# Optimization experiments

Hardware: AMD Instinct MI355X
Metric: run time of the kernel (lower is better)

Reference implementation:

```python
import jax, jax.numpy as jnp
import numpy as np

N_NODES = 50000
N_EDGES = 800000
IN_CH = 64
EDGE_DIM = 8
HIDDEN = 128
NUM_GRAPHS = 256


def setup_inputs() -> dict:
    key = jax.random.key(0)
    ks = jax.random.split(key, 16)
    x = jax.random.normal(ks[0], (N_NODES, IN_CH), dtype=jnp.float32)
    edge_index = jax.random.randint(ks[1], (2, N_EDGES), 0, N_NODES, dtype=jnp.int64)
    edge_attr = jax.random.normal(ks[2], (N_EDGES, EDGE_DIM), dtype=jnp.float32)
    batch = jnp.sort(jax.random.randint(ks[3], (N_NODES,), 0, NUM_GRAPHS, dtype=jnp.int64))

    def lin(k, fan_in, fan_out):
        bound = 1.0 / np.sqrt(fan_in)
        kw, kb = jax.random.split(k)
        W = jax.random.uniform(kw, (fan_in, fan_out), minval=-bound, maxval=bound, dtype=jnp.float32)
        b = jax.random.uniform(kb, (fan_out,), minval=-bound, maxval=bound, dtype=jnp.float32)
        return W, b

    W1, b1 = lin(ks[4], IN_CH, HIDDEN)
    We1, be1 = lin(ks[5], EDGE_DIM, IN_CH)
    W2, b2 = lin(ks[6], HIDDEN, HIDDEN)
    We2, be2 = lin(ks[7], EDGE_DIM, HIDDEN)
    W3, b3 = lin(ks[8], HIDDEN, HIDDEN)
    We3, be3 = lin(ks[9], EDGE_DIM, HIDDEN)
    return {"x": x, "edge_index": edge_index, "edge_attr": edge_attr, "batch": batch,
            "W1": W1, "b1": b1, "We1": We1, "be1": be1,
            "W2": W2, "b2": b2, "We2": We2, "be2": be2,
            "W3": W3, "b3": b3, "We3": We3, "be3": be3}


def gine_conv(x, src, dst, edge_attr, W, b, We, be):
    # edge feature projection to node-feature dim, then message = relu(x_j + e)
    e = edge_attr @ We + be                      # [E, d]
    msg = jax.nn.relu(x[src] + e)                # [E, d]
    agg = jax.ops.segment_sum(msg, dst, num_segments=x.shape[0])  # [N, d]
    # eps = 0 (PyG default, not trainable)
    return (x + agg) @ W + b


def reference(x, edge_index, edge_attr, batch,
              W1, b1, We1, be1, W2, b2, We2, be2, W3, b3, We3, be3):
    x = x.astype(jnp.float32)
    edge_attr = edge_attr.astype(jnp.float32)
    src, dst = edge_index[0], edge_index[1]
    x = jax.nn.relu(gine_conv(x, src, dst, edge_attr, W1, b1, We1, be1))
    x = jax.nn.relu(gine_conv(x, src, dst, edge_attr, W2, b2, We2, be2))
    x = jax.nn.relu(gine_conv(x, src, dst, edge_attr, W3, b3, We3, be3))
    # global mean pool over graphs
    sums = jax.ops.segment_sum(x, batch, num_segments=NUM_GRAPHS)          # [G, d]
    counts = jax.ops.segment_sum(jnp.ones((x.shape[0],), x.dtype), batch, num_segments=NUM_GRAPHS)
    return sums / jnp.maximum(counts, 1.0)[:, None]
```

## Files before the change

### kernel.cpp

```cpp
#include <hip/hip_runtime.h>
#include <hip/hip_bf16.h>
#include <hip/hip_fp16.h>

#define N_NODES 50000
#define N_EDGES 800000
#define IN_CH 64
#define EDGE_DIM 8
#define HIDDEN 128
#define NUM_GRAPHS 256
#define QSCALE 256.0f
#define QINV   (1.0f / 256.0f)

typedef __attribute__((ext_vector_type(8))) _Float16 half8;
typedef __attribute__((ext_vector_type(4))) float floatx4;
typedef __attribute__((ext_vector_type(2))) float floatx2;
typedef __attribute__((ext_vector_type(4))) int intx4;

static __device__ __forceinline__ __half2 u2h(int u) {
    union { int i; __half2 h; } cv; cv.i = u; return cv.h;
}
static __device__ __forceinline__ int h2u(__half2 h) {
    union { __half2 h; int i; } cv; cv.h = h; return cv.i;
}
static __device__ __forceinline__ unsigned short h1u(__half h) {
    union { __half h; unsigned short u; } cv; cv.h = h; return cv.u;
}
static __device__ __forceinline__ unsigned char f32_to_fp8(float v) {
    int pk = __builtin_amdgcn_cvt_pk_fp8_f32(v, v, 0, false);
    return (unsigned char)(pk & 0xff);
}

#define XH_ELEMS (N_NODES * IN_CH)

__global__ __launch_bounds__(256) void hist_cvt_kernel(
    const int* __restrict__ dst, int* __restrict__ deg,
    const float* __restrict__ x, unsigned char* __restrict__ xh8,
    const float* __restrict__ W1, const float* __restrict__ W2,
    const float* __restrict__ W3,
    _Float16* __restrict__ Wt1, _Float16* __restrict__ Wt2,
    _Float16* __restrict__ Wt3, int E)
{
    int i = blockIdx.x * blockDim.x + threadIdx.x;
    if (i < E) atomicAdd(&deg[dst[i]], 1);
    int idx = i;
    if (idx < XH_ELEMS) { xh8[idx] = f32_to_fp8(x[idx]); return; }
    idx -= XH_ELEMS;
    if (idx < 128 * IN_CH) {
        int n = idx / IN_CH, k = idx - n * IN_CH;
        Wt1[idx] = (_Float16)W1[k * 128 + n];
        return;
    }
    idx -= 128 * IN_CH;
    if (idx < 128 * HIDDEN) {
        int n = idx / HIDDEN, k = idx - n * HIDDEN;
        Wt2[idx] = (_Float16)W2[k * 128 + n];
        return;
    }
    idx -= 128 * HIDDEN;
    if (idx < 128 * HIDDEN) {
        int n = idx / HIDDEN, k = idx - n * HIDDEN;
        Wt3[idx] = (_Float16)W3[k * 128 + n];
    }
}

__global__ __launch_bounds__(256) void scan1_kernel(
    const int* __restrict__ deg, int* __restrict__ incl,
    int* __restrict__ blockSums, int N)
{
    __shared__ int s[256];
    int b = blockIdx.x, t = threadIdx.x;
    int i0 = b * 512 + 2 * t;
    int a0 = (i0 < N) ? deg[i0] : 0;
    int a1 = (i0 + 1 < N) ? deg[i0 + 1] : 0;
    int ps = a0 + a1;
    s[t] = ps;
    __syncthreads();
    for (int off = 1; off < 256; off <<= 1) {
        int v = (t >= off) ? s[t - off] : 0;
        __syncthreads();
        s[t] += v;
        __syncthreads();
    }
    int exclp = s[t] - ps;
    if (i0 < N)     incl[i0]     = exclp + a0;
    if (i0 + 1 < N) incl[i0 + 1] = exclp + a0 + a1;
    if (t == 255) blockSums[b] = s[255];
}

__global__ __launch_bounds__(128) void scan2_kernel(int* __restrict__ blockSums, int B)
{
    __shared__ int s[128];
    int t = threadIdx.x;
    int v = (t < B) ? blockSums[t] : 0;
    s[t] = v;
    __syncthreads();
    for (int off = 1; off < 128; off <<= 1) {
        int u = (t >= off) ? s[t - off] : 0;
        __syncthreads();
        s[t] += u;
        __syncthreads();
    }
    if (t < B) blockSums[t] = s[t] - v;
}

__global__ __launch_bounds__(256) void scan3_kernel(
    const int* __restrict__ incl, const int* __restrict__ deg,
    const int* __restrict__ blockSums, int* __restrict__ rowptr,
    int* __restrict__ pos, int N)
{
    int i = blockIdx.x * blockDim.x + threadIdx.x;
    if (i >= N) return;
    int v = incl[i] - deg[i] + blockSums[i >> 9];
    rowptr[i] = v;
    pos[i] = v;
}

__global__ __launch_bounds__(256) void scatter_rec_kernel(
    const int* __restrict__ dst, const int* __restrict__ src,
    const float* __restrict__ ea, int* __restrict__ pos,
    int* __restrict__ src_s, __half* __restrict__ ea16, int E)
{
    int e = blockIdx.x * blockDim.x + threadIdx.x;
    if (e >= E) return;
    int d = dst[e];
    int p = atomicAdd(&pos[d], 1);
    __builtin_nontemporal_store(src[e], &src_s[p]);
    const float4* q = (const float4*)(ea + (size_t)e * EDGE_DIM);
    float4 a = q[0], b = q[1];
    intx4 r;
    r.x = h2u(__floats2half2_rn(a.x, a.y));
    r.y = h2u(__floats2half2_rn(a.z, a.w));
    r.z = h2u(__floats2half2_rn(b.x, b.y));
    r.w = h2u(__floats2half2_rn(b.z, b.w));
    __builtin_nontemporal_store(r, (intx4*)(ea16 + (size_t)p * EDGE_DIM));
}

#define BF 8

__global__ __launch_bounds__(256) void gather_xs128_kernel(
    const unsigned char* __restrict__ h8,
    const int*    __restrict__ src_s,
    const __half* __restrict__ ea16,
    const int*    __restrict__ rowptr,
    const int*    __restrict__ deg,
    const float*  __restrict__ We,
    const float*  __restrict__ be,
    __half*       __restrict__ xs,
    int N)
{
    int wave = threadIdx.x >> 6;
    int n    = blockIdx.x * 4 + wave;
    if (n >= N) return;
    int l  = threadIdx.x & 63;
    int j0 = 2 * l;

    __half2 hw[8];
    #pragma unroll
    for (int k = 0; k < 8; ++k) {
        float2 wv = *(const float2*)&We[k * 128 + j0];
        hw[k] = __floats2half2_rn(wv.x, wv.y);
    }
    float2 bevf = *(const float2*)&be[j0];
    __half2 bev2 = __floats2half2_rn(bevf.x, bevf.y);

    int start = __builtin_amdgcn_readfirstlane(rowptr[n]);
    int dg    = __builtin_amdgcn_readfirstlane(deg[n]);

    unsigned short selfraw = *(const unsigned short*)&h8[(size_t)n * 128 + j0];
    floatx2 hf = __builtin_amdgcn_cvt_pk_f32_fp8((int)selfraw, false);
    int acci0 = 0, acci1 = 0;

    int nb = dg / BF;
    int base = start;
    for (int b = 0; b < nb; ++b, base += BF) {
        int sid[BF];
        #pragma unroll
        for (int t = 0; t < BF; ++t)
            sid[t] = __builtin_amdgcn_readfirstlane(
                __builtin_nontemporal_load(&src_s[base + t]));
        unsigned short hraw[BF];
        #pragma unroll
        for (int t = 0; t < BF; ++t)
            hraw[t] = *(const unsigned short*)&h8[(size_t)sid[t] * 128 + j0];
        intx4 eav[BF];
        #pragma unroll
        for (int t = 0; t < BF; ++t)
            eav[t] = __builtin_nontemporal_load(
                (const intx4*)&ea16[(size_t)(base + t) * 8]);

        #pragma unroll
        for (int t = 0; t < BF; ++t) {
            __half2 e01 = u2h(eav[t].x), e23 = u2h(eav[t].y);
            __half2 e45 = u2h(eav[t].z), e67 = u2h(eav[t].w);
            __half2 m = __hfma2(__low2half2(e01),  hw[0], bev2);
            m = __hfma2(__high2half2(e01), hw[1], m);
            m = __hfma2(__low2half2(e23),  hw[2], m);
            m = __hfma2(__high2half2(e23), hw[3], m);
            m = __hfma2(__low2half2(e45),  hw[4], m);
            m = __hfma2(__high2half2(e45), hw[5], m);
            m = __hfma2(__low2half2(e67),  hw[6], m);
            m = __hfma2(__high2half2(e67), hw[7], m);
            floatx2 hs = __builtin_amdgcn_cvt_pk_f32_fp8((int)hraw[t], false);
            float m0 = __half2float(__low2half(m))  + hs.x;
            float m1 = __half2float(__high2half(m)) + hs.y;
            acci0 += (int)((m0 > 0.0f ? m0 : 0.0f) * QSCALE);
            acci1 += (int)((m1 > 0.0f ? m1 : 0.0f) * QSCALE);
        }
    }
    int end = start + dg;
    for (int idx = base; idx < end; ++idx) {
        int s = __builtin_amdgcn_readfirstlane(src_s[idx]);
        unsigned short hr = *(const unsigned short*)&h8[(size_t)s * 128 + j0];
        intx4 ev = __builtin_nontemporal_load((const intx4*)&ea16[(size_t)idx * 8]);
        __half2 e01 = u2h(ev.x), e23 = u2h(ev.y), e45 = u2h(ev.z), e67 = u2h(ev.w);
        __half2 m = __hfma2(__low2half2(e01),  hw[0], bev2);
        m = __hfma2(__high2half2(e01), hw[1], m);
        m = __hfma2(__low2half2(e23),  hw[2], m);
        m = __hfma2(__high2half2(e23), hw[3], m);
        m = __hfma2(__low2half2(e45),  hw[4], m);
        m = __hfma2(__high2half2(e45), hw[5], m);
        m = __hfma2(__low2half2(e67),  hw[6], m);
        m = __hfma2(__high2half2(e67), hw[7], m);
        floatx2 hs = __builtin_amdgcn_cvt_pk_f32_fp8((int)hr, false);
        float m0 = __half2float(__low2half(m))  + hs.x;
        float m1 = __half2float(__high2half(m)) + hs.y;
        acci0 += (int)((m0 > 0.0f ? m0 : 0.0f) * QSCALE);
        acci1 += (int)((m1 > 0.0f ? m1 : 0.0f) * QSCALE);
    }
    float acc0 = hf.x + (float)acci0 * QINV;
    float acc1 = hf.y + (float)acci1 * QINV;
    __builtin_nontemporal_store(h2u(__floats2half2_rn(acc0, acc1)),
                                (int*)&xs[(size_t)n * 128 + j0]);
}

__global__ __launch_bounds__(256) void gather_xs64_kernel(
    const unsigned char* __restrict__ h8,
    const int*    __restrict__ src_s,
    const __half* __restrict__ ea16,
    const int*    __restrict__ rowptr,
    const int*    __restrict__ deg,
    const float*  __restrict__ We,
    const float*  __restrict__ be,
    __half*       __restrict__ xs,
    int N)
{
    int wave = threadIdx.x >> 6;
    int n    = blockIdx.x * 4 + wave;
    if (n >= N) return;
    int j = threadIdx.x & 63;

    __half2 w2[4];
    #pragma unroll
    for (int p = 0; p < 4; ++p)
        w2[p] = __floats2half2_rn(We[(2 * p) * 64 + j], We[(2 * p + 1) * 64 + j]);
    float bej = be[j];

    int start = __builtin_amdgcn_readfirstlane(rowptr[n]);
    int dg    = __builtin_amdgcn_readfirstlane(deg[n]);

    float selff = __builtin_amdgcn_cvt_f32_fp8((int)h8[(size_t)n * 64 + j], 0);
    int acci = 0;

    int nb = dg / BF;
    int base = start;
    for (int b = 0; b < nb; ++b, base += BF) {
        int sid[BF];
        #pragma unroll
        for (int t = 0; t < BF; ++t)
            sid[t] = __builtin_amdgcn_readfirstlane(
                __builtin_nontemporal_load(&src_s[base + t]));
        unsigned char hraw[BF];
        #pragma unroll
        for (int t = 0; t < BF; ++t)
            hraw[t] = h8[(size_t)sid[t] * 64 + j];
        intx4 eav[BF];
        #pragma unroll
        for (int t = 0; t < BF; ++t)
            eav[t] = __builtin_nontemporal_load(
                (const intx4*)&ea16[(size_t)(base + t) * 8]);

        #pragma unroll
        for (int t = 0; t < BF; ++t) {
            __half2 d = __hmul2(u2h(eav[t].x), w2[0]);
            d = __hfma2(u2h(eav[t].y), w2[1], d);
            d = __hfma2(u2h(eav[t].z), w2[2], d);
            d = __hfma2(u2h(eav[t].w), w2[3], d);
            float proj = __half2float(__low2half(d)) + __half2float(__high2half(d));
            float hrf = __builtin_amdgcn_cvt_f32_fp8((int)hraw[t], 0);
            float m = hrf + proj + bej;
            acci += (int)((m > 0.0f ? m : 0.0f) * QSCALE);
        }
    }
    int end = start + dg;
    for (int idx = base; idx < end; ++idx) {
        int s = __builtin_amdgcn_readfirstlane(src_s[idx]);
        float hrf = __builtin_amdgcn_cvt_f32_fp8((int)h8[(size_t)s * 64 + j], 0);
        intx4 ev = __builtin_nontemporal_load((const intx4*)&ea16[(size_t)idx * 8]);
        __half2 d = __hmul2(u2h(ev.x), w2[0]);
        d = __hfma2(u2h(ev.y), w2[1], d);
        d = __hfma2(u2h(ev.z), w2[2], d);
        d = __hfma2(u2h(ev.w), w2[3], d);
        float proj = __half2float(__low2half(d)) + __half2float(__high2half(d));
        float m = hrf + proj + bej;
        acci += (int)((m > 0.0f ? m : 0.0f) * QSCALE);
    }
    float acc = selff + (float)acci * QINV;
    __builtin_nontemporal_store(h1u(__float2half(acc)),
                                (unsigned short*)&xs[(size_t)n * 64 + j]);
}

template<int K, bool OUT8>
__global__ __launch_bounds__(256) void node_mfma_kernel(
    const _Float16* __restrict__ xs,
    const _Float16* __restrict__ Wt,
    const float*    __restrict__ b,
    _Float16*       __restrict__ out16,
    unsigned char*  __restrict__ out8,
    int N)
{
    int wave  = threadIdx.x >> 6;
    int lane  = threadIdx.x & 63;
    int row16 = lane & 15;
    int quad  = lane >> 4;
    int m0    = (blockIdx.x * 4 + wave) * 32;

    int nA = m0 + row16;        if (nA >= N) nA = N - 1;
    int nB = m0 + 16 + row16;   if (nB >= N) nB = N - 1;

    floatx4 accA[8], accB[8];
    #pragma unroll
    for (int t = 0; t < 8; ++t) { accA[t] = (floatx4)(0.0f); accB[t] = (floatx4)(0.0f); }

    #pragma unroll
    for (int kc = 0; kc < K; kc += 32) {
        half8 a0 = __builtin_nontemporal_load((const half8*)&xs[(size_t)nA * K + kc + quad * 8]);
        half8 a1 = __builtin_nontemporal_load((const half8*)&xs[(size_t)nB * K + kc + quad * 8]);
        #pragma unroll
        for (int t = 0; t < 8; ++t) {
            half8 bf = *(const half8*)&Wt[(size_t)(t * 16 + row16) * K + kc + quad * 8];
            accA[t] = __builtin_amdgcn_mfma_f32_16x16x32_f16(a0, bf, accA[t], 0, 0, 0);
            accB[t] = __builtin_amdgcn_mfma_f32_16x16x32_f16(a1, bf, accB[t], 0, 0, 0);
        }
    }

    #pragma unroll
    for (int t = 0; t < 8; ++t) {
        int col = t * 16 + row16;
        float bj = b[col];
        #pragma unroll
        for (int r = 0; r < 4; ++r) {
            int nodeA = m0 + quad * 4 + r;
            if (nodeA < N) {
                float v = accA[t][r] + bj;
                v = v > 0.0f ? v : 0.0f;
                if (OUT8) out8[(size_t)nodeA * 128 + col] = f32_to_fp8(v);
                else      out16[(size_t)nodeA * 128 + col] = (_Float16)v;
            }
            int nodeB = m0 + 16 + quad * 4 + r;
            if (nodeB < N) {
                float v = accB[t][r] + bj;
                v = v > 0.0f ? v : 0.0f;
                if (OUT8) out8[(size_t)nodeB * 128 + col] = f32_to_fp8(v);
                else      out16[(size_t)nodeB * 128 + col] = (_Float16)v;
            }
        }
    }
}

__global__ __launch_bounds__(256) void pool_kernel(
    const __half* __restrict__ h,
    const int*    __restrict__ batch,
    float*        __restrict__ out,
    int N)
{
    __shared__ int s_lo, s_hi;
    __shared__ float part[4][128];
    int g  = blockIdx.x;
    int t  = threadIdx.x;
    int fp = t & 63;
    int r  = t >> 6;

    if (t == 0) {
        int lo = 0, hi = N;
        while (lo < hi) { int m = (lo + hi) >> 1; if (batch[m] < g) lo = m + 1; else hi = m; }
        s_lo = lo;
        int lo2 = lo, hi2 = N;
        while (lo2 < hi2) { int m = (lo2 + hi2) >> 1; if (batch[m] < g + 1) lo2 = m + 1; else hi2 = m; }
        s_hi = lo2;
    }
    __syncthreads();

    int lo = s_lo, hi = s_hi;
    float a0 = 0.0f, a1 = 0.0f;
    for (int n = lo + r; n < hi; n += 4) {
        float2 f = __half22float2(*(const __half2*)&h[(size_t)n * 128 + 2 * fp]);
        a0 += f.x; a1 += f.y;
    }
    part[r][2 * fp]     = a0;
    part[r][2 * fp + 1] = a1;
    __syncthreads();

    if (r == 0) {
        float s0 = part[0][2 * fp] + part[1][2 * fp] + part[2][2 * fp] + part[3][2 * fp];
        float s1 = part[0][2 * fp + 1] + part[1][2 * fp + 1] + part[2][2 * fp + 1] + part[3][2 * fp + 1];
        float c = (float)(hi - lo);
        float d = c > 1.0f ? c : 1.0f;
        out[g * HIDDEN + 2 * fp]     = s0 / d;
        out[g * HIDDEN + 2 * fp + 1] = s1 / d;
    }
}

extern "C" void kernel_launch(void* const* d_in, const int* in_sizes, int n_in,
                              void* d_out, int out_size, void* d_ws, size_t ws_size,
                              hipStream_t stream)
{
    const float* x   = (const float*)d_in[0];
    const int*   ei  = (const int*)d_in[1];
    const float* ea  = (const float*)d_in[2];
    const int*   bat = (const int*)d_in[3];
    const float* W1  = (const float*)d_in[4];
    const float* b1  = (const float*)d_in[5];
    const float* We1 = (const float*)d_in[6];
    const float* be1 = (const float*)d_in[7];
    const float* W2  = (const float*)d_in[8];
    const float* b2  = (const float*)d_in[9];
    const float* We2 = (const float*)d_in[10];
    const float* be2 = (const float*)d_in[11];
    const float* W3  = (const float*)d_in[12];
    const float* b3  = (const float*)d_in[13];
    const float* We3 = (const float*)d_in[14];
    const float* be3 = (const float*)d_in[15];
    float* out = (float*)d_out;

    const int* src = ei;
    const int* dst = ei + N_EDGES;

    int* deg       = (int*)d_ws;
    int* rowptr    = deg + N_NODES;
    int* pos       = rowptr + N_NODES;
    int* src_s     = pos + N_NODES;
    int* blockSums = src_s + N_EDGES;
    __half* ea16   = (__half*)(blockSums + 128);
    __half* xs     = ea16 + (size_t)N_EDGES * EDGE_DIM;
    __half* h3h    = xs + (size_t)N_NODES * HIDDEN;
    unsigned char* xh8  = (unsigned char*)(h3h + (size_t)N_NODES * HIDDEN);
    unsigned char* h1_8 = xh8 + (size_t)N_NODES * IN_CH;
    unsigned char* h2_8 = h1_8 + (size_t)N_NODES * HIDDEN;
    _Float16* Wt1  = (_Float16*)(h2_8 + (size_t)N_NODES * HIDDEN);
    _Float16* Wt2  = Wt1 + 128 * IN_CH;
    _Float16* Wt3  = Wt2 + 128 * HIDDEN;

    const int BLK = 256;
    const int NB_E = (N_EDGES + BLK - 1) / BLK;
    const int NB_N = (N_NODES + BLK - 1) / BLK;
    const int SCAN_B = (N_NODES + 511) / 512;
    const int MFMA_B = (N_NODES + 127) / 128;
    const int WAVE4_B = (N_NODES + 3) / 4;
    const int CVT_ELEMS = XH_ELEMS + 128 * IN_CH + 2 * 128 * HIDDEN;
    const int NB_HC = (CVT_ELEMS + BLK - 1) / BLK;

    (void)hipMemsetAsync(deg, 0, N_NODES * sizeof(int), stream);
    hist_cvt_kernel<<<NB_HC, BLK, 0, stream>>>(
        dst, deg, x, xh8, W1, W2, W3, Wt1, Wt2, Wt3, N_EDGES);
    scan1_kernel<<<SCAN_B, 256, 0, stream>>>(deg, pos, blockSums, N_NODES);
    scan2_kernel<<<1, 128, 0, stream>>>(blockSums, SCAN_B);
    scan3_kernel<<<NB_N, BLK, 0, stream>>>(pos, deg, blockSums, rowptr, pos, N_NODES);
    scatter_rec_kernel<<<NB_E, BLK, 0, stream>>>(
        dst, src, ea, pos, src_s, ea16, N_EDGES);

    gather_xs64_kernel<<<WAVE4_B, BLK, 0, stream>>>(
        xh8, src_s, ea16, rowptr, deg, We1, be1, xs, N_NODES);
    node_mfma_kernel<IN_CH, true><<<MFMA_B, 256, 0, stream>>>(
        (const _Float16*)xs, Wt1, b1, nullptr, h1_8, N_NODES);

    gather_xs128_kernel<<<WAVE4_B, BLK, 0, stream>>>(
        h1_8, src_s, ea16, rowptr, deg, We2, be2, xs, N_NODES);
    node_mfma_kernel<HIDDEN, true><<<MFMA_B, 256, 0, stream>>>(
        (const _Float16*)xs, Wt2, b2, nullptr, h2_8, N_NODES);

    gather_xs128_kernel<<<WAVE4_B, BLK, 0, stream>>>(
        h2_8, src_s, ea16, rowptr, deg, We3, be3, xs, N_NODES);
    node_mfma_kernel<HIDDEN, false><<<MFMA_B, 256, 0, stream>>>(
        (const _Float16*)xs, Wt3, b3, (_Float16*)h3h, nullptr, N_NODES);

    pool_kernel<<<NUM_GRAPHS, 256, 0, stream>>>(h3h, bat, out, N_NODES);
}
```

Before: 416.4 us.

## Replace CSR build and node-gather with edge-parallel atomic scatter aggregation

Drops the degree histogram, three-kernel prefix scan and sort-by-destination scatter. Each layer now processes edges in original order and adds quantized messages into zeroed fixed-point accumulators with global atomics. For 128-wide layers it packs two 32-bit channel sums into one 64-bit atomic. The MFMA kernel adds the self term and dequantizes while loading its A operand. This removes the preprocessing kernels but moves the cost into many contended random atomics, plus a larger memset of the accumulator buffers.

```diff
diff --git a/kernel.cpp b/kernel.cpp
--- a/kernel.cpp
+++ b/kernel.cpp
@@ -15,15 +15,13 @@
 typedef __attribute__((ext_vector_type(4))) float floatx4;
 typedef __attribute__((ext_vector_type(2))) float floatx2;
 typedef __attribute__((ext_vector_type(4))) int intx4;
+typedef unsigned long long ull;
 
 static __device__ __forceinline__ __half2 u2h(int u) {
     union { int i; __half2 h; } cv; cv.i = u; return cv.h;
 }
 static __device__ __forceinline__ int h2u(__half2 h) {
     union { __half2 h; int i; } cv; cv.h = h; return cv.i;
-}
-static __device__ __forceinline__ unsigned short h1u(__half h) {
-    union { __half h; unsigned short u; } cv; cv.h = h; return cv.u;
 }
 static __device__ __forceinline__ unsigned char f32_to_fp8(float v) {
     int pk = __builtin_amdgcn_cvt_pk_fp8_f32(v, v, 0, false);
@@ -31,18 +29,17 @@
 }
 
 #define XH_ELEMS (N_NODES * IN_CH)
-
-__global__ __launch_bounds__(256) void hist_cvt_kernel(
-    const int* __restrict__ dst, int* __restrict__ deg,
+#define CVT_ELEMS (XH_ELEMS + 128 * IN_CH + 2 * 128 * HIDDEN + N_EDGES * EDGE_DIM)
+
+__global__ __launch_bounds__(256) void cvt_all_kernel(
     const float* __restrict__ x, unsigned char* __restrict__ xh8,
     const float* __restrict__ W1, const float* __restrict__ W2,
     const float* __restrict__ W3,
     _Float16* __restrict__ Wt1, _Float16* __restrict__ Wt2,
-    _Float16* __restrict__ Wt3, int E)
-{
-    int i = blockIdx.x * blockDim.x + threadIdx.x;
-    if (i < E) atomicAdd(&deg[dst[i]], 1);
-    int idx = i;
+    _Float16* __restrict__ Wt3,
+    const float* __restrict__ ea, __half* __restrict__ ea16)
+{
+    int idx = blockIdx.x * blockDim.x + threadIdx.x;
     if (idx < XH_ELEMS) { xh8[idx] = f32_to_fp8(x[idx]); return; }
     idx -= XH_ELEMS;
     if (idx < 128 * IN_CH) {
@@ -60,98 +57,28 @@
     if (idx < 128 * HIDDEN) {
         int n = idx / HIDDEN, k = idx - n * HIDDEN;
         Wt3[idx] = (_Float16)W3[k * 128 + n];
-    }
-}
-
-__global__ __launch_bounds__(256) void scan1_kernel(
-    const int* __restrict__ deg, int* __restrict__ incl,
-    int* __restrict__ blockSums, int N)
-{
-    __shared__ int s[256];
-    int b = blockIdx.x, t = threadIdx.x;
-    int i0 = b * 512 + 2 * t;
-    int a0 = (i0 < N) ? deg[i0] : 0;
-    int a1 = (i0 + 1 < N) ? deg[i0 + 1] : 0;
-    int ps = a0 + a1;
-    s[t] = ps;
-    __syncthreads();
-    for (int off = 1; off < 256; off <<= 1) {
-        int v = (t >= off) ? s[t - off] : 0;
-        __syncthreads();
-        s[t] += v;
-        __syncthreads();
-    }
-    int exclp = s[t] - ps;
-    if (i0 < N)     incl[i0]     = exclp + a0;
-    if (i0 + 1 < N) incl[i0 + 1] = exclp + a0 + a1;
-    if (t == 255) blockSums[b] = s[255];
-}
-
-__global__ __launch_bounds__(128) void scan2_kernel(int* __restrict__ blockSums, int B)
-{
-    __shared__ int s[128];
-    int t = threadIdx.x;
-    int v = (t < B) ? blockSums[t] : 0;
-    s[t] = v;
-    __syncthreads();
-    for (int off = 1; off < 128; off <<= 1) {
-        int u = (t >= off) ? s[t - off] : 0;
-        __syncthreads();
-        s[t] += u;
-        __syncthreads();
-    }
-    if (t < B) blockSums[t] = s[t] - v;
-}
-
-__global__ __launch_bounds__(256) void scan3_kernel(
-    const int* __restrict__ incl, const int* __restrict__ deg,
-    const int* __restrict__ blockSums, int* __restrict__ rowptr,
-    int* __restrict__ pos, int N)
-{
-    int i = blockIdx.x * blockDim.x + threadIdx.x;
-    if (i >= N) return;
-    int v = incl[i] - deg[i] + blockSums[i >> 9];
-    rowptr[i] = v;
-    pos[i] = v;
-}
-
-__global__ __launch_bounds__(256) void scatter_rec_kernel(
-    const int* __restrict__ dst, const int* __restrict__ src,
-    const float* __restrict__ ea, int* __restrict__ pos,
-    int* __restrict__ src_s, __half* __restrict__ ea16, int E)
-{
-    int e = blockIdx.x * blockDim.x + threadIdx.x;
-    if (e >= E) return;
-    int d = dst[e];
-    int p = atomicAdd(&pos[d], 1);
-    __builtin_nontemporal_store(src[e], &src_s[p]);
-    const float4* q = (const float4*)(ea + (size_t)e * EDGE_DIM);
-    float4 a = q[0], b = q[1];
-    intx4 r;
-    r.x = h2u(__floats2half2_rn(a.x, a.y));
-    r.y = h2u(__floats2half2_rn(a.z, a.w));
-    r.z = h2u(__floats2half2_rn(b.x, b.y));
-    r.w = h2u(__floats2half2_rn(b.z, b.w));
-    __builtin_nontemporal_store(r, (intx4*)(ea16 + (size_t)p * EDGE_DIM));
-}
-
-#define BF 8
-
-__global__ __launch_bounds__(256) void gather_xs128_kernel(
+        return;
+    }
+    idx -= 128 * HIDDEN;
+    if (idx < N_EDGES * EDGE_DIM)
+        ea16[idx] = __float2half(ea[idx]);
+}
+
+#define EB 8
+
+__global__ __launch_bounds__(256) void edge_add128_kernel(
+    const int* __restrict__ srcv, const int* __restrict__ dstv,
+    const __half* __restrict__ ea16,
     const unsigned char* __restrict__ h8,
-    const int*    __restrict__ src_s,
-    const __half* __restrict__ ea16,
-    const int*    __restrict__ rowptr,
-    const int*    __restrict__ deg,
-    const float*  __restrict__ We,
-    const float*  __restrict__ be,
-    __half*       __restrict__ xs,
-    int N)
+    const float* __restrict__ We,
+    const float* __restrict__ be,
+    ull* __restrict__ xsi,
+    int E)
 {
     int wave = threadIdx.x >> 6;
-    int n    = blockIdx.x * 4 + wave;
-    if (n >= N) return;
-    int l  = threadIdx.x & 63;
+    int l    = threadIdx.x & 63;
+    int base = (blockIdx.x * 4 + wave) * EB;
+    if (base >= E) return;
     int j0 = 2 * l;
 
     __half2 hw[8];
@@ -163,33 +90,32 @@
     float2 bevf = *(const float2*)&be[j0];
     __half2 bev2 = __floats2half2_rn(bevf.x, bevf.y);
 
-    int start = __builtin_amdgcn_readfirstlane(rowptr[n]);
-    int dg    = __builtin_amdgcn_readfirstlane(deg[n]);
-
-    unsigned short selfraw = *(const unsigned short*)&h8[(size_t)n * 128 + j0];
-    floatx2 hf = __builtin_amdgcn_cvt_pk_f32_fp8((int)selfraw, false);
-    int acci0 = 0, acci1 = 0;
-
-    int nb = dg / BF;
-    int base = start;
-    for (int b = 0; b < nb; ++b, base += BF) {
-        int sid[BF];
-        #pragma unroll
-        for (int t = 0; t < BF; ++t)
-            sid[t] = __builtin_amdgcn_readfirstlane(
-                __builtin_nontemporal_load(&src_s[base + t]));
-        unsigned short hraw[BF];
-        #pragma unroll
-        for (int t = 0; t < BF; ++t)
-            hraw[t] = *(const unsigned short*)&h8[(size_t)sid[t] * 128 + j0];
-        intx4 eav[BF];
-        #pragma unroll
-        for (int t = 0; t < BF; ++t)
-            eav[t] = __builtin_nontemporal_load(
-                (const intx4*)&ea16[(size_t)(base + t) * 8]);
-
-        #pragma unroll
-        for (int t = 0; t < BF; ++t) {
+    int cnt = E - base; if (cnt > EB) cnt = EB;
+
+    int sid[EB], did[EB];
+    unsigned short hraw[EB];
+    intx4 eav[EB];
+    #pragma unroll
+    for (int t = 0; t < EB; ++t) {
+        int tt = t < cnt ? t : cnt - 1;
+        sid[t] = __builtin_amdgcn_readfirstlane(
+            __builtin_nontemporal_load(&srcv[base + tt]));
+        did[t] = __builtin_amdgcn_readfirstlane(
+            __builtin_nontemporal_load(&dstv[base + tt]));
+    }
+    #pragma unroll
+    for (int t = 0; t < EB; ++t)
+        hraw[t] = *(const unsigned short*)&h8[(size_t)sid[t] * 128 + j0];
+    #pragma unroll
+    for (int t = 0; t < EB; ++t) {
+        int tt = t < cnt ? t : cnt - 1;
+        eav[t] = __builtin_nontemporal_load(
+            (const intx4*)&ea16[(size_t)(base + tt) * 8]);
+    }
+
+    #pragma unroll
+    for (int t = 0; t < EB; ++t) {
+        if (t < cnt) {
             __half2 e01 = u2h(eav[t].x), e23 = u2h(eav[t].y);
             __half2 e45 = u2h(eav[t].z), e67 = u2h(eav[t].w);
             __half2 m = __hfma2(__low2half2(e01),  hw[0], bev2);
@@ -203,51 +129,27 @@
             floatx2 hs = __builtin_amdgcn_cvt_pk_f32_fp8((int)hraw[t], false);
             float m0 = __half2float(__low2half(m))  + hs.x;
             float m1 = __half2float(__high2half(m)) + hs.y;
-            acci0 += (int)((m0 > 0.0f ? m0 : 0.0f) * QSCALE);
-            acci1 += (int)((m1 > 0.0f ? m1 : 0.0f) * QSCALE);
-        }
-    }
-    int end = start + dg;
-    for (int idx = base; idx < end; ++idx) {
-        int s = __builtin_amdgcn_readfirstlane(src_s[idx]);
-        unsigned short hr = *(const unsigned short*)&h8[(size_t)s * 128 + j0];
-        intx4 ev = __builtin_nontemporal_load((const intx4*)&ea16[(size_t)idx * 8]);
-        __half2 e01 = u2h(ev.x), e23 = u2h(ev.y), e45 = u2h(ev.z), e67 = u2h(ev.w);
-        __half2 m = __hfma2(__low2half2(e01),  hw[0], bev2);
-        m = __hfma2(__high2half2(e01), hw[1], m);
-        m = __hfma2(__low2half2(e23),  hw[2], m);
-        m = __hfma2(__high2half2(e23), hw[3], m);
-        m = __hfma2(__low2half2(e45),  hw[4], m);
-        m = __hfma2(__high2half2(e45), hw[5], m);
-        m = __hfma2(__low2half2(e67),  hw[6], m);
-        m = __hfma2(__high2half2(e67), hw[7], m);
-        floatx2 hs = __builtin_amdgcn_cvt_pk_f32_fp8((int)hr, false);
-        float m0 = __half2float(__low2half(m))  + hs.x;
-        float m1 = __half2float(__high2half(m)) + hs.y;
-        acci0 += (int)((m0 > 0.0f ? m0 : 0.0f) * QSCALE);
-        acci1 += (int)((m1 > 0.0f ? m1 : 0.0f) * QSCALE);
-    }
-    float acc0 = hf.x + (float)acci0 * QINV;
-    float acc1 = hf.y + (float)acci1 * QINV;
-    __builtin_nontemporal_store(h2u(__floats2half2_rn(acc0, acc1)),
-                                (int*)&xs[(size_t)n * 128 + j0]);
-}
-
-__global__ __launch_bounds__(256) void gather_xs64_kernel(
+            unsigned q0 = (unsigned)(int)((m0 > 0.0f ? m0 : 0.0f) * QSCALE);
+            unsigned q1 = (unsigned)(int)((m1 > 0.0f ? m1 : 0.0f) * QSCALE);
+            ull v = ((ull)q1 << 32) | (ull)q0;
+            if (v) atomicAdd(&xsi[(size_t)did[t] * 64 + l], v);
+        }
+    }
+}
+
+__global__ __launch_bounds__(256) void edge_add64_kernel(
+    const int* __restrict__ srcv, const int* __restrict__ dstv,
+    const __half* __restrict__ ea16,
     const unsigned char* __restrict__ h8,
-    const int*    __restrict__ src_s,
-    const __half* __restrict__ ea16,
-    const int*    __restrict__ rowptr,
-    const int*    __restrict__ deg,
-    const float*  __restrict__ We,
-    const float*  __restrict__ be,
-    __half*       __restrict__ xs,
-    int N)
+    const float* __restrict__ We,
+    const float* __restrict__ be,
+    unsigned* __restrict__ xsi,
+    int E)
 {
     int wave = threadIdx.x >> 6;
-    int n    = blockIdx.x * 4 + wave;
-    if (n >= N) return;
-    int j = threadIdx.x & 63;
+    int j    = threadIdx.x & 63;
+    int base = (blockIdx.x * 4 + wave) * EB;
+    if (base >= E) return;
 
     __half2 w2[4];
     #pragma unroll
@@ -255,32 +157,32 @@
         w2[p] = __floats2half2_rn(We[(2 * p) * 64 + j], We[(2 * p + 1) * 64 + j]);
     float bej = be[j];
 
-    int start = __builtin_amdgcn_readfirstlane(rowptr[n]);
-    int dg    = __builtin_amdgcn_readfirstlane(deg[n]);
-
-    float selff = __builtin_amdgcn_cvt_f32_fp8((int)h8[(size_t)n * 64 + j], 0);
-    int acci = 0;
-
-    int nb = dg / BF;
-    int base = start;
-    for (int b = 0; b < nb; ++b, base += BF) {
-        int sid[BF];
-        #pragma unroll
-        for (int t = 0; t < BF; ++t)
-            sid[t] = __builtin_amdgcn_readfirstlane(
-                __builtin_nontemporal_load(&src_s[base + t]));
-        unsigned char hraw[BF];
-        #pragma unroll
-        for (int t = 0; t < BF; ++t)
-            hraw[t] = h8[(size_t)sid[t] * 64 + j];
-        intx4 eav[BF];
-        #pragma unroll
-        for (int t = 0; t < BF; ++t)
-            eav[t] = __builtin_nontemporal_load(
-                (const intx4*)&ea16[(size_t)(base + t) * 8]);
-
-        #pragma unroll
-        for (int t = 0; t < BF; ++t) {
+    int cnt = E - base; if (cnt > EB) cnt = EB;
+
+    int sid[EB], did[EB];
+    unsigned char hraw[EB];
+    intx4 eav[EB];
+    #pragma unroll
+    for (int t = 0; t < EB; ++t) {
+        int tt = t < cnt ? t : cnt - 1;
+        sid[t] = __builtin_amdgcn_readfirstlane(
+            __builtin_nontemporal_load(&srcv[base + tt]));
+        did[t] = __builtin_amdgcn_readfirstlane(
+            __builtin_nontemporal_load(&dstv[base + tt]));
+    }
+    #pragma unroll
+    for (int t = 0; t < EB; ++t)
+        hraw[t] = h8[(size_t)sid[t] * 64 + j];
+    #pragma unroll
+    for (int t = 0; t < EB; ++t) {
+        int tt = t < cnt ? t : cnt - 1;
+        eav[t] = __builtin_nontemporal_load(
+            (const intx4*)&ea16[(size_t)(base + tt) * 8]);
+    }
+
+    #pragma unroll
+    for (int t = 0; t < EB; ++t) {
+        if (t < cnt) {
             __half2 d = __hmul2(u2h(eav[t].x), w2[0]);
             d = __hfma2(u2h(eav[t].y), w2[1], d);
             d = __hfma2(u2h(eav[t].z), w2[2], d);
@@ -288,30 +190,16 @@
             float proj = __half2float(__low2half(d)) + __half2float(__high2half(d));
             float hrf = __builtin_amdgcn_cvt_f32_fp8((int)hraw[t], 0);
             float m = hrf + proj + bej;
-            acci += (int)((m > 0.0f ? m : 0.0f) * QSCALE);
-        }
-    }
-    int end = start + dg;
-    for (int idx = base; idx < end; ++idx) {
-        int s = __builtin_amdgcn_readfirstlane(src_s[idx]);
-        float hrf = __builtin_amdgcn_cvt_f32_fp8((int)h8[(size_t)s * 64 + j], 0);
-        intx4 ev = __builtin_nontemporal_load((const intx4*)&ea16[(size_t)idx * 8]);
-        __half2 d = __hmul2(u2h(ev.x), w2[0]);
-        d = __hfma2(u2h(ev.y), w2[1], d);
-        d = __hfma2(u2h(ev.z), w2[2], d);
-        d = __hfma2(u2h(ev.w), w2[3], d);
-        float proj = __half2float(__low2half(d)) + __half2float(__high2half(d));
-        float m = hrf + proj + bej;
-        acci += (int)((m > 0.0f ? m : 0.0f) * QSCALE);
-    }
-    float acc = selff + (float)acci * QINV;
-    __builtin_nontemporal_store(h1u(__float2half(acc)),
-                                (unsigned short*)&xs[(size_t)n * 64 + j]);
+            unsigned q = (unsigned)(int)((m > 0.0f ? m : 0.0f) * QSCALE);
+            if (q) atomicAdd(&xsi[(size_t)did[t] * 64 + j], q);
+        }
+    }
 }
 
 template<int K, bool OUT8>
 __global__ __launch_bounds__(256) void node_mfma_kernel(
-    const _Float16* __restrict__ xs,
+    const void*     __restrict__ xsi_v,
+    const unsigned char* __restrict__ h8,
     const _Float16* __restrict__ Wt,
     const float*    __restrict__ b,
     _Float16*       __restrict__ out16,
@@ -333,8 +221,38 @@
 
     #pragma unroll
     for (int kc = 0; kc < K; kc += 32) {
-        half8 a0 = __builtin_nontemporal_load((const half8*)&xs[(size_t)nA * K + kc + quad * 8]);
-        half8 a1 = __builtin_nontemporal_load((const half8*)&xs[(size_t)nB * K + kc + quad * 8]);
+        int off = kc + quad * 8;
+        half8 a0, a1;
+        if constexpr (K == 64) {
+            const unsigned* xrA = (const unsigned*)xsi_v + (size_t)nA * 64 + off;
+            const unsigned* xrB = (const unsigned*)xsi_v + (size_t)nB * 64 + off;
+            const unsigned short* hpA = (const unsigned short*)(h8 + (size_t)nA * 64 + off);
+            const unsigned short* hpB = (const unsigned short*)(h8 + (size_t)nB * 64 + off);
+            #pragma unroll
+            for (int p = 0; p < 4; ++p) {
+                floatx2 hsA = __builtin_amdgcn_cvt_pk_f32_fp8((int)hpA[p], false);
+                floatx2 hsB = __builtin_amdgcn_cvt_pk_f32_fp8((int)hpB[p], false);
+                a0[2 * p]     = (_Float16)(hsA.x + (float)(int)xrA[2 * p]     * QINV);
+                a0[2 * p + 1] = (_Float16)(hsA.y + (float)(int)xrA[2 * p + 1] * QINV);
+                a1[2 * p]     = (_Float16)(hsB.x + (float)(int)xrB[2 * p]     * QINV);
+                a1[2 * p + 1] = (_Float16)(hsB.y + (float)(int)xrB[2 * p + 1] * QINV);
+            }
+        } else {
+            const ull* xrA = (const ull*)xsi_v + (size_t)nA * 64 + off / 2;
+            const ull* xrB = (const ull*)xsi_v + (size_t)nB * 64 + off / 2;
+            const unsigned short* hpA = (const unsigned short*)(h8 + (size_t)nA * 128 + off);
+            const unsigned short* hpB = (const unsigned short*)(h8 + (size_t)nB * 128 + off);
+            #pragma unroll
+            for (int p = 0; p < 4; ++p) {
+                ull vA = xrA[p], vB = xrB[p];
+                floatx2 hsA = __builtin_amdgcn_cvt_pk_f32_fp8((int)hpA[p], false);
+                floatx2 hsB = __builtin_amdgcn_cvt_pk_f32_fp8((int)hpB[p], false);
+                a0[2 * p]     = (_Float16)(hsA.x + (float)(int)(unsigned)(vA & 0xffffffffull) * QINV);
+                a0[2 * p + 1] = (_Float16)(hsA.y + (float)(int)(unsigned)(vA >> 32) * QINV);
+                a1[2 * p]     = (_Float16)(hsB.x + (float)(int)(unsigned)(vB & 0xffffffffull) * QINV);
+                a1[2 * p + 1] = (_Float16)(hsB.y + (float)(int)(unsigned)(vB >> 32) * QINV);
+            }
+        }
         #pragma unroll
         for (int t = 0; t < 8; ++t) {
             half8 bf = *(const half8*)&Wt[(size_t)(t * 16 + row16) * K + kc + quad * 8];
@@ -435,14 +353,11 @@
     const int* src = ei;
     const int* dst = ei + N_EDGES;
 
-    int* deg       = (int*)d_ws;
-    int* rowptr    = deg + N_NODES;
-    int* pos       = rowptr + N_NODES;
-    int* src_s     = pos + N_NODES;
-    int* blockSums = src_s + N_EDGES;
-    __half* ea16   = (__half*)(blockSums + 128);
-    __half* xs     = ea16 + (size_t)N_EDGES * EDGE_DIM;
-    __half* h3h    = xs + (size_t)N_NODES * HIDDEN;
+    ull*      xsiA = (ull*)d_ws;
+    ull*      xsiB = xsiA + (size_t)N_NODES * 64;
+    unsigned* xsi1 = (unsigned*)(xsiB + (size_t)N_NODES * 64);
+    __half* ea16   = (__half*)(xsi1 + (size_t)N_NODES * 64);
+    __half* h3h    = ea16 + (size_t)N_EDGES * EDGE_DIM;
     unsigned char* xh8  = (unsigned char*)(h3h + (size_t)N_NODES * HIDDEN);
     unsigned char* h1_8 = xh8 + (size_t)N_NODES * IN_CH;
     unsigned char* h2_8 = h1_8 + (size_t)N_NODES * HIDDEN;
@@ -451,37 +366,30 @@
     _Float16* Wt3  = Wt2 + 128 * HIDDEN;
 
     const int BLK = 256;
-    const int NB_E = (N_EDGES + BLK - 1) / BLK;
-    const int NB_N = (N_NODES + BLK - 1) / BLK;
-    const int SCAN_B = (N_NODES + 511) / 512;
     const int MFMA_B = (N_NODES + 127) / 128;
-    const int WAVE4_B = (N_NODES + 3) / 4;
-    const int CVT_ELEMS = XH_ELEMS + 128 * IN_CH + 2 * 128 * HIDDEN;
-    const int NB_HC = (CVT_ELEMS + BLK - 1) / BLK;
-
-    (void)hipMemsetAsync(deg, 0, N_NODES * sizeof(int), stream);
-    hist_cvt_kernel<<<NB_HC, BLK, 0, stream>>>(
-        dst, deg, x, xh8, W1, W2, W3, Wt1, Wt2, Wt3, N_EDGES);
-    scan1_kernel<<<SCAN_B, 256, 0, stream>>>(deg, pos, blockSums, N_NODES);
-    scan2_kernel<<<1, 128, 0, stream>>>(blockSums, SCAN_B);
-    scan3_kernel<<<NB_N, BLK, 0, stream>>>(pos, deg, blockSums, rowptr, pos, N_NODES);
-    scatter_rec_kernel<<<NB_E, BLK, 0, stream>>>(
-        dst, src, ea, pos, src_s, ea16, N_EDGES);
-
-    gather_xs64_kernel<<<WAVE4_B, BLK, 0, stream>>>(
-        xh8, src_s, ea16, rowptr, deg, We1, be1, xs, N_NODES);
+    const int EDGE_B = (N_EDGES + 4 * EB - 1) / (4 * EB);
+    const int NB_CVT = (CVT_ELEMS + BLK - 1) / BLK;
+
+    const size_t ZERO_BYTES = (size_t)N_NODES * 64 * (8 + 8 + 4);
+
+    (void)hipMemsetAsync(xsiA, 0, ZERO_BYTES, stream);
+    cvt_all_kernel<<<NB_CVT, BLK, 0, stream>>>(
+        x, xh8, W1, W2, W3, Wt1, Wt2, Wt3, ea, ea16);
+
+    edge_add64_kernel<<<EDGE_B, BLK, 0, stream>>>(
+        src, dst, ea16, xh8, We1, be1, xsi1, N_EDGES);
     node_mfma_kernel<IN_CH, true><<<MFMA_B, 256, 0, stream>>>(
-        (const _Float16*)xs, Wt1, b1, nullptr, h1_8, N_NODES);
-
-    gather_xs128_kernel<<<WAVE4_B, BLK, 0, stream>>>(
-        h1_8, src_s, ea16, rowptr, deg, We2, be2, xs, N_NODES);
+        (const void*)xsi1, xh8, Wt1, b1, nullptr, h1_8, N_NODES);
+
+    edge_add128_kernel<<<EDGE_B, BLK, 0, stream>>>(
+        src, dst, ea16, h1_8, We2, be2, xsiA, N_EDGES);
     node_mfma_kernel<HIDDEN, true><<<MFMA_B, 256, 0, stream>>>(
-        (const _Float16*)xs, Wt2, b2, nullptr, h2_8, N_NODES);
-
-    gather_xs128_kernel<<<WAVE4_B, BLK, 0, stream>>>(
-        h2_8, src_s, ea16, rowptr, deg, We3, be3, xs, N_NODES);
+        (const void*)xsiA, h1_8, Wt2, b2, nullptr, h2_8, N_NODES);
+
+    edge_add128_kernel<<<EDGE_B, BLK, 0, stream>>>(
+        src, dst, ea16, h2_8, We3, be3, xsiB, N_EDGES);
     node_mfma_kernel<HIDDEN, false><<<MFMA_B, 256, 0, stream>>>(
-        (const _Float16*)xs, Wt3, b3, (_Float16*)h3h, nullptr, N_NODES);
+        (const void*)xsiB, h2_8, Wt3, b3, (_Float16*)h3h, nullptr, N_NODES);
 
     pool_kernel<<<NUM_GRAPHS, 256, 0, stream>>>(h3h, bat, out, N_NODES);
 }
```

Result: slower. 906.6 us (+117.8%).
